# Kernel optimization log

Hardware: AMD Instinct MI355X
Metric: run time of the kernel (lower is better)

## Reference

```python
import jax, jax.numpy as jnp
import numpy as np

B, T, D, H = 16, 2048, 1024, 1024  # batch, seq (effective block_size), n_embed, head_size


def setup_inputs() -> dict:
    key = jax.random.key(0)
    k1, k2, k3, k4 = jax.random.split(key, 4)
    x = jax.random.normal(k1, (B, T, D), dtype=jnp.float32)
    # torch Linear weight is [out,in]; store as [in,out] for x @ W
    s = 1.0 / np.sqrt(D)
    Wq = jax.random.uniform(k2, (D, H), dtype=jnp.float32, minval=-s, maxval=s)
    Wk = jax.random.uniform(k3, (D, H), dtype=jnp.float32, minval=-s, maxval=s)
    Wv = jax.random.uniform(k4, (D, H), dtype=jnp.float32, minval=-s, maxval=s)
    return {"x": x, "Wq": Wq, "Wk": Wk, "Wv": Wv}


def reference(x, Wq, Wk, Wv):
    # Single-head causal self-attention, NO 1/sqrt(d) scaling (faithful to source).
    q = x @ Wq  # [B,T,H]
    k = x @ Wk  # [B,T,H]
    v = x @ Wv  # [B,T,H]
    w = jnp.einsum('bth,bsh->bts', q, k)  # [B,T,T]
    Tn = x.shape[1]
    causal = jnp.tril(jnp.ones((Tn, Tn), dtype=bool))
    w = jnp.where(causal, w, -jnp.inf)
    w = jax.nn.softmax(w, axis=-1)
    # dropout is identity in eval mode
    out = jnp.einsum('bts,bsh->bth', w, v)  # [B,T,H]
    return out
```

## Files before the change

### kernel.cpp

```cpp
#include <hip/hip_runtime.h>
#include <hip/hip_bf16.h>


typedef _Float16 half8 __attribute__((ext_vector_type(8)));
typedef _Float16 half4v __attribute__((ext_vector_type(4)));
typedef float floatx4 __attribute__((ext_vector_type(4)));

#define TB 16
#define TT 2048
#define TD 1024

__global__ void cvt_f32_f16(const float* __restrict__ in, _Float16* __restrict__ out, long n) {
    long i = ((long)blockIdx.x * blockDim.x + threadIdx.x) * 4;
    long stride = (long)gridDim.x * blockDim.x * 4;
    for (; i < n; i += stride) {
        float4 f = *(const float4*)(in + i);
        half4v h;
        h[0] = (_Float16)f.x; h[1] = (_Float16)f.y;
        h[2] = (_Float16)f.z; h[3] = (_Float16)f.w;
        *(half4v*)(out + i) = h;
    }
}

__global__ void transpose_cvt_w(const float* __restrict__ in, _Float16* __restrict__ out) {
    __shared__ float tile[32][33];
    const int bx = blockIdx.x * 32, by = blockIdx.y * 32;
    const int tx = threadIdx.x, ty = threadIdx.y;
#pragma unroll
    for (int i = ty; i < 32; i += 8) tile[i][tx] = in[(long)(by + i) * 1024 + bx + tx];
    __syncthreads();
#pragma unroll
    for (int i = ty; i < 32; i += 8) out[(long)(bx + i) * 1024 + by + tx] = (_Float16)tile[tx][i];
}

__device__ __forceinline__ void gload16(const _Float16* g, _Float16* l) {
    __builtin_amdgcn_global_load_lds((const __attribute__((address_space(1))) void*)g,
                                     (__attribute__((address_space(3))) void*)l, 16, 0, 0);
}

template <int MODE>
__global__ __launch_bounds__(512, 2) void gemm256(const _Float16* __restrict__ A,
                                                  const _Float16* __restrict__ B,
                                                  void* __restrict__ Cout,
                                                  void* __restrict__ Cout2,
                                                  int K, int lda, int ldb, int ldc,
                                                  long sAb, long sBb, long sCb,
                                                  int tilesN, int tilesM, int nb) {
    __shared__ _Float16 lds[65536];
    const int tid = threadIdx.x, lane = tid & 63, w = tid >> 6;
    const int wr = w >> 2, wc = w & 3;

    int b, ti, tj;
    if (MODE == 2) {
        const int grp = nb * 4;
        const int g = blockIdx.x / grp;
        ti = tilesM - 1 - g;
        int i2 = blockIdx.x - g * grp;
        const int q = grp >> 3, r = grp & 7, xcd = i2 & 7, idx = i2 >> 3;
        i2 = (xcd < r ? xcd * (q + 1) : r * (q + 1) + (xcd - r) * q) + idx;
        b = i2 >> 2; tj = i2 & 3;
    } else {
        int bx = blockIdx.x;
        const int nwg = gridDim.x, q = nwg >> 3, r = nwg & 7, xcd = bx & 7, idx = bx >> 3;
        bx = (xcd < r ? xcd * (q + 1) : r * (q + 1) + (xcd - r) * q) + idx;
        b = blockIdx.y;
        if (MODE == 1) {
            int rd = bx; ti = 0;
            while (rd > ti) { rd -= ti + 1; ++ti; }
            tj = rd;
        } else {
            ti = bx / tilesN; tj = bx % tilesN;
        }
    }
    A += (long)b * sAb;
    B += (long)b * sBb;
    const long m0 = (long)ti * 256, n0 = (long)tj * 256;
    const int nkt = (MODE == 2) ? (ti + 1) * 4 : (K >> 6);

    const int row0 = tid >> 2;
    const int co   = (((tid & 3) ^ ((tid >> 3) & 3)) << 3);
    const int fcol = ((((lane >> 4) ^ (lane >> 1)) & 3) << 3);
    const int arow = wr * 128 + (lane & 15);
    const int brow = wc * 64 + (lane & 15);

    auto Abase = [&](int buf, int kk) { return lds + ((buf * 2 + kk) << 13); };
    auto Bbase = [&](int buf, int kk) { return lds + 32768 + ((buf * 2 + kk) << 13); };

    auto stageA = [&](int buf, int kk, int kt) {
        const long kb = (long)kt * 64 + kk * 32 + co;
        _Float16* d = Abase(buf, kk) + (w << 9);
        gload16(A + (m0 + row0) * (long)lda + kb, d);
        gload16(A + (m0 + row0 + 128) * (long)lda + kb, d + 4096);
    };
    auto stageB = [&](int buf, int kk, int kt) {
        const long kb = (long)kt * 64 + kk * 32 + co;
        _Float16* d = Bbase(buf, kk) + (w << 9);
        gload16(B + (n0 + row0) * (long)ldb + kb, d);
        gload16(B + (n0 + row0 + 128) * (long)ldb + kb, d + 4096);
    };
    auto ldA = [&](int buf, int kk, int m) {
        return *(const half8*)(Abase(buf, kk) + (arow + m * 16) * 32 + fcol);
    };
    auto ldB = [&](int buf, int kk, int n) {
        return *(const half8*)(Bbase(buf, kk) + (brow + n * 16) * 32 + fcol);
    };

    floatx4 acc[8][4] = {};

#define MFMA16(MH)                                                                     \
    _Pragma("unroll") for (int mm = 0; mm < 4; ++mm)                                   \
    _Pragma("unroll") for (int nn = 0; nn < 4; ++nn)                                   \
        acc[(MH)*4 + mm][nn] =                                                         \
            __builtin_amdgcn_mfma_f32_16x16x32_f16(afr[mm], bfr[nn], acc[(MH)*4 + mm][nn], 0, 0, 0);

    stageA(0, 0, 0); stageB(0, 0, 0); stageA(0, 1, 0); stageB(0, 1, 0);
    asm volatile("s_waitcnt vmcnt(4)" ::: "memory");
    __builtin_amdgcn_s_barrier();

    for (int t = 0; t < nkt; ++t) {
        const int cur = t & 1, nxt = cur ^ 1;
        const bool pf = (t + 1 < nkt);
        const int kn = t + 1;
        half8 afr[4], bfr[4];
#pragma unroll
        for (int nn = 0; nn < 4; ++nn) bfr[nn] = ldB(cur, 0, nn);
#pragma unroll
        for (int mm = 0; mm < 4; ++mm) afr[mm] = ldA(cur, 0, mm);
        if (pf) stageA(nxt, 0, kn);
        __builtin_amdgcn_s_barrier();
        asm volatile("s_waitcnt lgkmcnt(0)" ::: "memory");
        __builtin_amdgcn_sched_barrier(0);
        __builtin_amdgcn_s_setprio(1);
        MFMA16(0)
        __builtin_amdgcn_s_setprio(0);
        __builtin_amdgcn_s_barrier();
#pragma unroll
        for (int mm = 0; mm < 4; ++mm) afr[mm] = ldA(cur, 0, mm + 4);
        if (pf) stageB(nxt, 0, kn);
        __builtin_amdgcn_s_barrier();
        asm volatile("s_waitcnt lgkmcnt(0)" ::: "memory");
        __builtin_amdgcn_sched_barrier(0);
        __builtin_amdgcn_s_setprio(1);
        MFMA16(1)
        __builtin_amdgcn_s_setprio(0);
        if (pf) { asm volatile("s_waitcnt vmcnt(4)" ::: "memory"); }
        else    { asm volatile("s_waitcnt vmcnt(0)" ::: "memory"); }
        __builtin_amdgcn_s_barrier();
#pragma unroll
        for (int nn = 0; nn < 4; ++nn) bfr[nn] = ldB(cur, 1, nn);
#pragma unroll
        for (int mm = 0; mm < 4; ++mm) afr[mm] = ldA(cur, 1, mm);
        if (pf) stageA(nxt, 1, kn);
        __builtin_amdgcn_s_barrier();
        asm volatile("s_waitcnt lgkmcnt(0)" ::: "memory");
        __builtin_amdgcn_sched_barrier(0);
        __builtin_amdgcn_s_setprio(1);
        MFMA16(0)
        __builtin_amdgcn_s_setprio(0);
        __builtin_amdgcn_s_barrier();
#pragma unroll
        for (int mm = 0; mm < 4; ++mm) afr[mm] = ldA(cur, 1, mm + 4);
        if (pf) stageB(nxt, 1, kn);
        __builtin_amdgcn_s_barrier();
        asm volatile("s_waitcnt lgkmcnt(0)" ::: "memory");
        __builtin_amdgcn_sched_barrier(0);
        __builtin_amdgcn_s_setprio(1);
        MFMA16(1)
        __builtin_amdgcn_s_setprio(0);
        asm volatile("s_waitcnt vmcnt(4)" ::: "memory");
        __builtin_amdgcn_s_barrier();
    }
#undef MFMA16

    const int r4 = (lane >> 4) * 4, ccol = lane & 15;
    if (MODE != 2) {
        _Float16* C;
        long nb0 = n0;
        if (MODE == 3 && n0 >= TD) { C = (_Float16*)Cout2; nb0 = n0 - TD; }
        else                        C = (_Float16*)Cout + (long)b * sCb;
#pragma unroll
        for (int m = 0; m < 8; ++m) {
            const long rbase = m0 + wr * 128 + m * 16 + r4;
#pragma unroll
            for (int n = 0; n < 4; ++n) {
                const long cbase = nb0 + wc * 64 + n * 16 + ccol;
#pragma unroll
                for (int j = 0; j < 4; ++j)
                    C[(rbase + j) * (long)ldc + cbase] = (_Float16)acc[m][n][j];
            }
        }
    } else {
        float* C = (float*)Cout + (long)b * sCb;
#pragma unroll
        for (int m = 0; m < 8; ++m) {
            const long rbase = m0 + wr * 128 + m * 16 + r4;
#pragma unroll
            for (int n = 0; n < 4; ++n) {
                const long cbase = n0 + wc * 64 + n * 16 + ccol;
#pragma unroll
                for (int j = 0; j < 4; ++j)
                    C[(rbase + j) * (long)ldc + cbase] = acc[m][n][j];
            }
        }
    }
}

__global__ __launch_bounds__(256) void softmax_rows_f16(_Float16* __restrict__ S, int T) {
    const int wv = threadIdx.x >> 6, lane = threadIdx.x & 63;
    const long row = (long)blockIdx.x * 4 + wv;
    const int t = (int)(row & (T - 1));
    _Float16* s = S + row * (long)T;
    const int nstore = ((t >> 8) + 1) << 8;

    float v[4][8];
    float mx = -__builtin_inff();
#pragma unroll
    for (int c = 0; c < 4; ++c) {
        const int col0 = (c * 64 + lane) * 8;
        if (col0 <= t) {
            half8 hv = *(const half8*)(s + col0);
#pragma unroll
            for (int j = 0; j < 8; ++j) {
                v[c][j] = (col0 + j <= t) ? (float)hv[j] : -__builtin_inff();
                mx = fmaxf(mx, v[c][j]);
            }
        } else {
#pragma unroll
            for (int j = 0; j < 8; ++j) v[c][j] = -__builtin_inff();
        }
    }
#pragma unroll
    for (int o = 32; o; o >>= 1) mx = fmaxf(mx, __shfl_xor(mx, o));

    float sum = 0.f;
#pragma unroll
    for (int c = 0; c < 4; ++c)
#pragma unroll
        for (int j = 0; j < 8; ++j) {
            float p = __expf(v[c][j] - mx);
            v[c][j] = p;
            sum += p;
        }
#pragma unroll
    for (int o = 32; o; o >>= 1) sum += __shfl_xor(sum, o);
    const float inv = 1.f / sum;

#pragma unroll
    for (int c = 0; c < 4; ++c) {
        const int col0 = (c * 64 + lane) * 8;
        if (col0 < nstore) {
            half8 o;
#pragma unroll
            for (int j = 0; j < 8; ++j) o[j] = (_Float16)(v[c][j] * inv);
            *(half8*)(s + col0) = o;
        }
    }
}

extern "C" void kernel_launch(void* const* d_in, const int* in_sizes, int n_in,
                              void* d_out, int out_size, void* d_ws, size_t ws_size,
                              hipStream_t stream) {
    const float* x  = (const float*)d_in[0];
    const float* Wq = (const float*)d_in[1];
    const float* Wk = (const float*)d_in[2];
    const float* Wv = (const float*)d_in[3];
    float* out = (float*)d_out;

    const size_t XB = (size_t)TB * TT * TD;

    _Float16* x16 = (_Float16*)d_out;
    _Float16* Kh  = (_Float16*)d_out + XB;

    char* ws = (char*)d_ws;
    size_t off = 0;
    auto carve = [&](size_t bytes) { char* p = ws + off; off = (off + bytes + 255) & ~(size_t)255; return p; };
    _Float16* wqt = (_Float16*)carve((size_t)TD * TD * 2);
    _Float16* wkt = (_Float16*)carve((size_t)TD * TD * 2);
    _Float16* wvt = (_Float16*)carve((size_t)TD * TD * 2);
    _Float16* Qh  = (_Float16*)carve(XB * 2);
    _Float16* Vt  = (_Float16*)carve(XB * 2);

    const size_t CH = (size_t)TT * TT * 2;
    int NB = 16;
    while (NB > 1 && off + (size_t)NB * CH > ws_size) NB >>= 1;
    _Float16* Sc = (_Float16*)carve((size_t)NB * CH);

    cvt_f32_f16<<<2048, 256, 0, stream>>>(x, x16, (long)XB);
    transpose_cvt_w<<<dim3(32, 32), dim3(32, 8), 0, stream>>>(Wq, wqt);
    transpose_cvt_w<<<dim3(32, 32), dim3(32, 8), 0, stream>>>(Wk, wkt);
    transpose_cvt_w<<<dim3(32, 32), dim3(32, 8), 0, stream>>>(Wv, wvt);

    gemm256<3><<<dim3(128 * 8, 1), 512, 0, stream>>>(x16, wqt, Qh, Kh, TD, TD, TD, TD,
                                                     0, 0, 0, 8, 128, 0);
    gemm256<0><<<dim3(4 * 8, TB), 512, 0, stream>>>(wvt, x16, Vt, nullptr, TD, TD, TD, TT,
                                                    0, (long)TT * TD, (long)TD * TT, 8, 4, 0);

    for (int cb = 0; cb < TB; cb += NB) {
        gemm256<1><<<dim3(36, NB), 512, 0, stream>>>(Qh + (size_t)cb * TT * TD,
                                                     Kh + (size_t)cb * TT * TD, Sc, nullptr,
                                                     TD, TD, TD, TT,
                                                     (long)TT * TD, (long)TT * TD, (long)TT * TT, 8, 8, 0);
        softmax_rows_f16<<<NB * TT / 4, 256, 0, stream>>>(Sc, TT);
        gemm256<2><<<dim3(NB * 32, 1), 512, 0, stream>>>(Sc, Vt + (size_t)cb * TD * TT,
                                                         out + (size_t)cb * TT * TD, nullptr, TT,
                                                         TT, TT, TD,
                                                         (long)TT * TT, (long)TD * TT, (long)TT * TD, 4, 8, NB);
    }
}
```

Baseline: 483.5 us.

## Double-buffer MFMA fragments and deepen global prefetch in GEMM main loop

Restructures the GEMM main loop so LDS fragment loads for the next quarter are issued while the current quarter's MFMAs run, using separate even/odd register fragment sets. Global prefetch is deepened to stage two k-tiles ahead, with clamped indices instead of conditional prefetch, and the number of barriers per iteration drops. This aims to hide LDS and global latency behind matrix math. In exchange it uses more registers, which can lower occupancy. The clamped indices also issue redundant loads on the final iterations.

```diff
diff --git a/kernel.cpp b/kernel.cpp
--- a/kernel.cpp
+++ b/kernel.cpp
@@ -106,71 +106,76 @@
     };
 
     floatx4 acc[8][4] = {};
-
-#define MFMA16(MH)                                                                     \
+    half8 afE[4], afO[4], bfE[4], bfO[4];
+
+#define MFMA_Q(MH, BF, AF)                                                             \
     _Pragma("unroll") for (int mm = 0; mm < 4; ++mm)                                   \
     _Pragma("unroll") for (int nn = 0; nn < 4; ++nn)                                   \
         acc[(MH)*4 + mm][nn] =                                                         \
-            __builtin_amdgcn_mfma_f32_16x16x32_f16(afr[mm], bfr[nn], acc[(MH)*4 + mm][nn], 0, 0, 0);
-
-    stageA(0, 0, 0); stageB(0, 0, 0); stageA(0, 1, 0); stageB(0, 1, 0);
-    asm volatile("s_waitcnt vmcnt(4)" ::: "memory");
+            __builtin_amdgcn_mfma_f32_16x16x32_f16(AF[mm], BF[nn], acc[(MH)*4 + mm][nn], 0, 0, 0);
+
+    {
+        const int k1 = (1 < nkt) ? 1 : nkt - 1;
+        stageA(0, 0, 0); stageB(0, 0, 0);
+        stageA(0, 1, 0); stageB(0, 1, 0);
+        stageA(1, 0, k1); stageB(1, 0, k1);
+    }
+    asm volatile("s_waitcnt vmcnt(8)" ::: "memory");
     __builtin_amdgcn_s_barrier();
+#pragma unroll
+    for (int nn = 0; nn < 4; ++nn) bfE[nn] = ldB(0, 0, nn);
+#pragma unroll
+    for (int mm = 0; mm < 4; ++mm) afE[mm] = ldA(0, 0, mm);
 
     for (int t = 0; t < nkt; ++t) {
         const int cur = t & 1, nxt = cur ^ 1;
-        const bool pf = (t + 1 < nkt);
-        const int kn = t + 1;
-        half8 afr[4], bfr[4];
-#pragma unroll
-        for (int nn = 0; nn < 4; ++nn) bfr[nn] = ldB(cur, 0, nn);
-#pragma unroll
-        for (int mm = 0; mm < 4; ++mm) afr[mm] = ldA(cur, 0, mm);
-        if (pf) stageA(nxt, 0, kn);
+        const int kt1 = (t + 1 < nkt) ? t + 1 : nkt - 1;
+        const int kt2 = (t + 2 < nkt) ? t + 2 : nkt - 1;
+        asm volatile("s_waitcnt lgkmcnt(0)" ::: "memory");
+        __builtin_amdgcn_sched_barrier(0);
+        __builtin_amdgcn_s_setprio(1);
+        MFMA_Q(0, bfE, afE)
+        __builtin_amdgcn_s_setprio(0);
+#pragma unroll
+        for (int mm = 0; mm < 4; ++mm) afO[mm] = ldA(cur, 0, mm + 4);
+        stageA(nxt, 1, kt1);
+        asm volatile("s_waitcnt vmcnt(6)" ::: "memory");
         __builtin_amdgcn_s_barrier();
         asm volatile("s_waitcnt lgkmcnt(0)" ::: "memory");
         __builtin_amdgcn_sched_barrier(0);
         __builtin_amdgcn_s_setprio(1);
-        MFMA16(0)
+        MFMA_Q(1, bfE, afO)
         __builtin_amdgcn_s_setprio(0);
-        __builtin_amdgcn_s_barrier();
-#pragma unroll
-        for (int mm = 0; mm < 4; ++mm) afr[mm] = ldA(cur, 0, mm + 4);
-        if (pf) stageB(nxt, 0, kn);
+#pragma unroll
+        for (int nn = 0; nn < 4; ++nn) bfO[nn] = ldB(cur, 1, nn);
+#pragma unroll
+        for (int mm = 0; mm < 4; ++mm) afE[mm] = ldA(cur, 1, mm);
+        stageB(nxt, 1, kt1);
         __builtin_amdgcn_s_barrier();
         asm volatile("s_waitcnt lgkmcnt(0)" ::: "memory");
         __builtin_amdgcn_sched_barrier(0);
         __builtin_amdgcn_s_setprio(1);
-        MFMA16(1)
+        MFMA_Q(0, bfO, afE)
         __builtin_amdgcn_s_setprio(0);
-        if (pf) { asm volatile("s_waitcnt vmcnt(4)" ::: "memory"); }
-        else    { asm volatile("s_waitcnt vmcnt(0)" ::: "memory"); }
-        __builtin_amdgcn_s_barrier();
-#pragma unroll
-        for (int nn = 0; nn < 4; ++nn) bfr[nn] = ldB(cur, 1, nn);
-#pragma unroll
-        for (int mm = 0; mm < 4; ++mm) afr[mm] = ldA(cur, 1, mm);
-        if (pf) stageA(nxt, 1, kn);
+#pragma unroll
+        for (int mm = 0; mm < 4; ++mm) afO[mm] = ldA(cur, 1, mm + 4);
+        stageA(cur, 0, kt2);
+        asm volatile("s_waitcnt vmcnt(6)" ::: "memory");
         __builtin_amdgcn_s_barrier();
         asm volatile("s_waitcnt lgkmcnt(0)" ::: "memory");
         __builtin_amdgcn_sched_barrier(0);
         __builtin_amdgcn_s_setprio(1);
-        MFMA16(0)
+        MFMA_Q(1, bfO, afO)
         __builtin_amdgcn_s_setprio(0);
+#pragma unroll
+        for (int nn = 0; nn < 4; ++nn) bfE[nn] = ldB(nxt, 0, nn);
+#pragma unroll
+        for (int mm = 0; mm < 4; ++mm) afE[mm] = ldA(nxt, 0, mm);
+        stageB(cur, 0, kt2);
         __builtin_amdgcn_s_barrier();
-#pragma unroll
-        for (int mm = 0; mm < 4; ++mm) afr[mm] = ldA(cur, 1, mm + 4);
-        if (pf) stageB(nxt, 1, kn);
-        __builtin_amdgcn_s_barrier();
-        asm volatile("s_waitcnt lgkmcnt(0)" ::: "memory");
-        __builtin_amdgcn_sched_barrier(0);
-        __builtin_amdgcn_s_setprio(1);
-        MFMA16(1)
-        __builtin_amdgcn_s_setprio(0);
-        asm volatile("s_waitcnt vmcnt(4)" ::: "memory");
-        __builtin_amdgcn_s_barrier();
-    }
-#undef MFMA16
+    }
+#undef MFMA_Q
+    asm volatile("s_waitcnt vmcnt(0) lgkmcnt(0)" ::: "memory");
 
     const int r4 = (lane >> 4) * 4, ccol = lane & 15;
     if (MODE != 2) {
```

New measurement: 472.4 us. 1.02x faster.
